# Kernel tuning notes

Hardware: AMD Instinct MI355X
Metric: run time of the kernel (lower is better)

Reference implementation:

```python
import jax, jax.numpy as jnp
import numpy as np

EMBED_DIM = 1024
NUM_HEADS = 16
HEAD_DIM = EMBED_DIM // NUM_HEADS


def setup_inputs() -> dict:
    key = jax.random.key(0)
    ks = jax.random.split(key, 9)
    B, S, E = 2, 2048, EMBED_DIM
    scale = 1.0 / np.sqrt(E)
    return {
        "query": jax.random.normal(ks[0], (B, S, E), jnp.float32),
        "key": jax.random.normal(ks[1], (B, S, E), jnp.float32),
        "value": jax.random.normal(ks[2], (B, S, E), jnp.float32),
        "wq": jax.random.normal(ks[3], (E, E), jnp.float32) * scale,
        "bq": jnp.zeros((E,), jnp.float32),
        "wk": jax.random.normal(ks[4], (E, E), jnp.float32) * scale,
        "bk": jnp.zeros((E,), jnp.float32),
        "wv": jax.random.normal(ks[5], (E, E), jnp.float32) * scale,
        "bv": jnp.zeros((E,), jnp.float32),
    }


def _split_heads(x):
    B, S, _ = x.shape
    return x.reshape(B, S, NUM_HEADS, HEAD_DIM).transpose(0, 2, 1, 3)  # [B,H,S,Dh]


def reference(query, key, value, wq, bq, wk, bk, wv, bv):
    q = _split_heads(query @ wq + bq)   # [B,H,S,Dh]
    k = _split_heads(key @ wk + bk)
    v = _split_heads(value @ wv + bv)
    logits = jnp.einsum("bhqd,bhkd->bhqk", q, k) / jnp.sqrt(
        jnp.asarray(HEAD_DIM, q.dtype)
    )
    attn = jax.nn.softmax(logits, axis=-1)          # [B,H,S,S]
    out = jnp.einsum("bhqk,bhkd->bhqd", attn, v)    # [B,H,S,Dh]
    B, H, S, Dh = out.shape
    out = out.transpose(0, 2, 1, 3).reshape(B, S, H * Dh)  # [B,S,E]
    return out, attn
```

## Files before the change

kernel.cpp:

```cpp
#include <hip/hip_runtime.h>

typedef float  f32x4   __attribute__((ext_vector_type(4)));
typedef float  f32x16  __attribute__((ext_vector_type(16)));
typedef int    i32x4   __attribute__((ext_vector_type(4)));
typedef short  bf16x8  __attribute__((ext_vector_type(8)));
typedef short  s16x4   __attribute__((ext_vector_type(4)));

#define NB   2
#define SEQ  2048
#define EMB  1024
#define NH   16
#define DH   64
#define MATN (NB * SEQ * EMB)

__device__ inline short f2bf(float f) {
    unsigned u = __float_as_uint(f);
    u += 0x7fffu + ((u >> 16) & 1u);
    return (short)(u >> 16);
}

__device__ inline unsigned cvtpk(float lo, float hi) {
    unsigned r;
    asm("v_cvt_pk_bf16_f32 %0, %1, %2" : "=v"(r) : "v"(lo), "v"(hi));
    return r;
}

__device__ inline float fexp2(float x) {
#if __has_builtin(__builtin_amdgcn_exp2f)
    return __builtin_amdgcn_exp2f(x);
#else
    return exp2f(x);
#endif
}

__device__ inline f32x4 mfma16(bf16x8 a, bf16x8 b, f32x4 c) {
    return __builtin_amdgcn_mfma_f32_16x16x32_bf16(a, b, c, 0, 0, 0);
}
__device__ inline f32x16 mfma32(bf16x8 a, bf16x8 b, f32x16 c) {
    return __builtin_amdgcn_mfma_f32_32x32x16_bf16(a, b, c, 0, 0, 0);
}

__device__ inline void gload_lds16(const short* g, short* l) {
    __builtin_amdgcn_global_load_lds(
        (const __attribute__((address_space(1))) void*)g,
        (__attribute__((address_space(3))) void*)l, 16, 0, 0);
}

__global__ __launch_bounds__(256) void prep_kernel(const float* __restrict__ q,
                                                   const float* __restrict__ k,
                                                   const float* __restrict__ v,
                                                   const float* __restrict__ w0,
                                                   const float* __restrict__ w1,
                                                   const float* __restrict__ w2,
                                                   short* __restrict__ wt,
                                                   short* __restrict__ abf) {
    int blk = blockIdx.x;
    int t = threadIdx.x;
    if (blk < 3072) {
        __shared__ float tile[32][33];
        int mat = blk >> 10;
        int rem = blk & 1023;
        int kt = rem >> 5, nt = rem & 31;
        const float* W = (mat == 0) ? w0 : ((mat == 1) ? w1 : w2);
        int row = t >> 3, c4 = (t & 7) << 2;

        f32x4 val = *(const f32x4*)(W + (kt * 32 + row) * EMB + nt * 32 + c4);
        tile[row][c4 + 0] = val[0];
        tile[row][c4 + 1] = val[1];
        tile[row][c4 + 2] = val[2];
        tile[row][c4 + 3] = val[3];
        __syncthreads();

        int n = nt * 32 + row;
        s16x4 o;
        o[0] = f2bf(tile[c4 + 0][row]);
        o[1] = f2bf(tile[c4 + 1][row]);
        o[2] = f2bf(tile[c4 + 2][row]);
        o[3] = f2bf(tile[c4 + 3][row]);
        *(s16x4*)(wt + mat * (EMB * EMB) + n * EMB + kt * 32 + c4) = o;
    } else {
        long long i = (long long)(blk - 3072) * 2048 + t * 8;
        int mat = (int)(i >> 22);
        int off = (int)(i & (MATN - 1));
        const float* A = (mat == 0) ? q : ((mat == 1) ? k : v);
        f32x4 x = *(const f32x4*)(A + off);
        f32x4 y = *(const f32x4*)(A + off + 4);
        bf16x8 pk;
        pk[0] = f2bf(x[0]); pk[1] = f2bf(x[1]); pk[2] = f2bf(x[2]); pk[3] = f2bf(x[3]);
        pk[4] = f2bf(y[0]); pk[5] = f2bf(y[1]); pk[6] = f2bf(y[2]); pk[7] = f2bf(y[3]);
        *(bf16x8*)(abf + i) = pk;
    }
}

template <bool BF16A>
__global__ __launch_bounds__(256) void proj_kernel(const short* __restrict__ abf,
                                                   const float* __restrict__ a0,
                                                   const float* __restrict__ a1,
                                                   const float* __restrict__ a2,
                                                   const float* __restrict__ b0,
                                                   const float* __restrict__ b1,
                                                   const float* __restrict__ b2,
                                                   const short* __restrict__ wt,
                                                   short* __restrict__ qkv) {
    __shared__ __align__(16) short smem[18432];

    int orig = blockIdx.x;
    int blk = (orig & 7) * 96 + (orig >> 3);
    int mat = blk >> 8;
    int rem = blk & 255;
    int mt = rem >> 3, nt = rem & 7;

    const float* bias = (mat == 0) ? b0 : ((mat == 1) ? b1 : b2);
    const float* Af = (mat == 0) ? a0 : ((mat == 1) ? a1 : a2);
    const short* Ab = abf + mat * MATN;
    const short* WT = wt + mat * (EMB * EMB);
    short* O = qkv + mat * MATN;
    float scale = (mat == 0) ? 0.125f * 1.44269504f : 1.0f;

    int t = threadIdx.x;
    int lane = t & 63, w = t >> 6;
    int wr = w >> 1, wc = w & 1;
    int lg = lane >> 4, lm = lane & 15;

    int m0 = mt * 128, n0 = nt * 128;

    f32x4 acc[4][4] = {};

    if constexpr (BF16A) {
        const short* gA[4];
        const short* gW[4];
        int ldso[4];
#pragma unroll
        for (int i = 0; i < 4; i++) {
            int u = w * 256 + i * 64 + lane;
            int row = u >> 3;
            int c = (u & 7) ^ (row & 7);
            gA[i] = Ab + (m0 + row) * EMB + c * 8;
            gW[i] = WT + (n0 + row) * EMB + c * 8;
            ldso[i] = (w * 256 + i * 64) * 8;
        }
        int xr = lm & 7;
        for (int k0 = 0; k0 < EMB; k0 += 64) {
#pragma unroll
            for (int i = 0; i < 4; i++) {
                gload_lds16(gA[i] + k0, smem + ldso[i]);
                gload_lds16(gW[i] + k0, smem + 8192 + ldso[i]);
            }
            __syncthreads();
#pragma unroll
            for (int ks = 0; ks < 2; ks++) {
                bf16x8 af[4], bfr[4];
                int cc = (ks * 4 + lg) ^ xr;
#pragma unroll
                for (int mi = 0; mi < 4; mi++)
                    af[mi] = *(const bf16x8*)(smem + (wr * 64 + mi * 16 + lm) * 64 + cc * 8);
#pragma unroll
                for (int ni = 0; ni < 4; ni++)
                    bfr[ni] = *(const bf16x8*)(smem + 8192 + (wc * 64 + ni * 16 + lm) * 64 + cc * 8);
#pragma unroll
                for (int mi = 0; mi < 4; mi++)
#pragma unroll
                    for (int ni = 0; ni < 4; ni++)
                        acc[mi][ni] = mfma16(af[mi], bfr[ni], acc[mi][ni]);
            }
            __syncthreads();
        }
    } else {
        int srow = t >> 1, koff = (t & 1) * 32;
        for (int k0 = 0; k0 < EMB; k0 += 64) {
            const float* ap = Af + (m0 + srow) * EMB + k0 + koff;
#pragma unroll
            for (int i = 0; i < 4; i++) {
                f32x4 x = *(const f32x4*)(ap + i * 8);
                f32x4 y = *(const f32x4*)(ap + i * 8 + 4);
                bf16x8 pk;
                pk[0] = f2bf(x[0]); pk[1] = f2bf(x[1]); pk[2] = f2bf(x[2]); pk[3] = f2bf(x[3]);
                pk[4] = f2bf(y[0]); pk[5] = f2bf(y[1]); pk[6] = f2bf(y[2]); pk[7] = f2bf(y[3]);
                *(bf16x8*)&smem[srow * 72 + koff + i * 8] = pk;
            }
            const short* wp = WT + (n0 + srow) * EMB + k0 + koff;
#pragma unroll
            for (int i = 0; i < 4; i++)
                *(i32x4*)&smem[9216 + srow * 72 + koff + i * 8] = *(const i32x4*)(wp + i * 8);
            __syncthreads();
#pragma unroll
            for (int ks = 0; ks < 2; ks++) {
                bf16x8 af[4], bfr[4];
#pragma unroll
                for (int mi = 0; mi < 4; mi++)
                    af[mi] = *(const bf16x8*)&smem[(wr * 64 + mi * 16 + lm) * 72 + ks * 32 + lg * 8];
#pragma unroll
                for (int ni = 0; ni < 4; ni++)
                    bfr[ni] = *(const bf16x8*)&smem[9216 + (wc * 64 + ni * 16 + lm) * 72 + ks * 32 + lg * 8];
#pragma unroll
                for (int mi = 0; mi < 4; mi++)
#pragma unroll
                    for (int ni = 0; ni < 4; ni++)
                        acc[mi][ni] = mfma16(af[mi], bfr[ni], acc[mi][ni]);
            }
            __syncthreads();
        }
    }

    int bidx = m0 >> 11;
    if (mat == 2) {
#pragma unroll
        for (int ni = 0; ni < 4; ni++) {
            int e = n0 + wc * 64 + ni * 16 + lm;
            float bv = bias[e];
            int h = e >> 6, d = e & 63;
#pragma unroll
            for (int mi = 0; mi < 4; mi++) {
                int s = (m0 + wr * 64 + mi * 16 + lg * 4) & (SEQ - 1);
                s16x4 o;
#pragma unroll
                for (int r = 0; r < 4; r++) o[r] = f2bf(acc[mi][ni][r] + bv);
                *(s16x4*)(O + (((bidx * NH + h) * DH + d) * SEQ) + s) = o;
            }
        }
    } else {
#pragma unroll
        for (int ni = 0; ni < 4; ni++) {
            int e = n0 + wc * 64 + ni * 16 + lm;
            float bv = bias[e];
#pragma unroll
            for (int mi = 0; mi < 4; mi++) {
                int rr = wr * 64 + mi * 16 + lg * 4;
#pragma unroll
                for (int r = 0; r < 4; r++)
                    smem[(rr + r) * 136 + wc * 64 + ni * 16 + lm] =
                        f2bf((acc[mi][ni][r] + bv) * scale);
            }
        }
        __syncthreads();
        int r = t >> 1, half = t & 1;
        int h = (n0 + half * 64) >> 6;
        int s = (m0 + r) & (SEQ - 1);
        short* dst = O + (((long long)bidx * NH + h) * SEQ + s) * DH;
        const short* srcp = smem + r * 136 + half * 64;
#pragma unroll
        for (int j = 0; j < 8; j++)
            *(i32x4*)(dst + j * 8) = *(const i32x4*)(srcp + j * 8);
    }
}

__global__ __launch_bounds__(256) void attn_kernel(const short* __restrict__ qkv,
                                                   float* __restrict__ out,
                                                   float* __restrict__ attn) {
    const short* Qb = qkv;
    const short* Kb = qkv + MATN;
    const short* Vt = qkv + 2 * MATN;

    __shared__ __align__(16) short kbuf[2][64][72];
    __shared__ __align__(16) short vbuf[2][4096];
    __shared__ float lds_rs[4][32];

    int orig = blockIdx.x;
    int wg = (orig & 7) * 128 + (orig >> 3);
    int bh = wg >> 5;
    int q0 = (wg & 31) * 64;
    int b = bh >> 4, hq = bh & 15;

    int t = threadIdx.x, lane = t & 63, w = t >> 6;
    int lg = lane >> 4, lm = lane & 15;
    int srow = t >> 2, sch = t & 3;

    const short* kbase = Kb + (long long)bh * SEQ * DH;
    const short* vbase = Vt + (long long)bh * DH * SEQ;

    bf16x8 qf0, qf1;
    {
        const short* qrow = Qb + ((long long)bh * SEQ + q0 + w * 16 + lm) * DH + lg * 8;
        qf0 = *(const bf16x8*)(qrow);
        qf1 = *(const bf16x8*)(qrow + 32);
    }

    int l31 = lane & 31, l5 = lane >> 5;
    int khalf = w >> 1;
    bf16x8 qw[4];
    {
        const short* qr = Qb + ((long long)bh * SEQ + q0 + (w & 1) * 32 + l31) * DH + l5 * 8;
        qw[0] = *(const bf16x8*)(qr);
        qw[1] = *(const bf16x8*)(qr + 16);
        qw[2] = *(const bf16x8*)(qr + 32);
        qw[3] = *(const bf16x8*)(qr + 48);
    }

    i32x4 kr0, kr1;
    {
        const short* kp = kbase + srow * DH + sch * 16;
        kr0 = *(const i32x4*)(kp); kr1 = *(const i32x4*)(kp + 8);
    }
    float rsum = 0.0f;
    for (int kt = 0; kt < 32; kt++) {
        *(i32x4*)&kbuf[kt & 1][srow][sch * 16]     = kr0;
        *(i32x4*)&kbuf[kt & 1][srow][sch * 16 + 8] = kr1;
        __syncthreads();
        if (kt < 31) {
            const short* kp = kbase + ((kt + 1) * 64 + srow) * DH + sch * 16;
            kr0 = *(const i32x4*)(kp); kr1 = *(const i32x4*)(kp + 8);
        }
        const short* kb = &kbuf[kt & 1][khalf * 32 + l31][l5 * 8];
        f32x16 s = {};
        __builtin_amdgcn_s_setprio(1);
        s = mfma32(*(const bf16x8*)(kb),      qw[0], s);
        s = mfma32(*(const bf16x8*)(kb + 16), qw[1], s);
        s = mfma32(*(const bf16x8*)(kb + 32), qw[2], s);
        s = mfma32(*(const bf16x8*)(kb + 48), qw[3], s);
        __builtin_amdgcn_s_setprio(0);
#pragma unroll
        for (int r = 0; r < 16; r++) rsum += fexp2(s[r]);
    }
    rsum += __shfl_xor(rsum, 32);
    if (lane < 32) lds_rs[w][lane] = rsum;
    __syncthreads();
    float ml2r;
    {
        int q = w * 16 + lm;
        float tot = (q < 32) ? (lds_rs[0][q] + lds_rs[2][q])
                             : (lds_rs[1][q - 32] + lds_rs[3][q - 32]);
        ml2r = -__log2f(tot);
    }

    f32x4 oacc[4] = {};
    float* arow = attn + ((long long)bh * SEQ + q0 + w * 16 + lm) * SEQ;

    int vA0 = (srow >> 4) * 1024 + (sch >> 1) * 512 + (srow & 15) * 8 + (sch & 1) * 4;

    i32x4 vr0, vr1;
    {
        const short* kp = kbase + srow * DH + sch * 16;
        kr0 = *(const i32x4*)(kp); kr1 = *(const i32x4*)(kp + 8);
        const short* vp = vbase + srow * SEQ + sch * 16;
        vr0 = *(const i32x4*)(vp); vr1 = *(const i32x4*)(vp + 8);
    }

    for (int kt = 0; kt < 32; kt++) {
        *(i32x4*)&kbuf[kt & 1][srow][sch * 16]     = kr0;
        *(i32x4*)&kbuf[kt & 1][srow][sch * 16 + 8] = kr1;
        union { i32x4 v; s16x4 h[2]; } u0, u1;
        u0.v = vr0; u1.v = vr1;
        *(s16x4*)&vbuf[kt & 1][vA0]       = u0.h[0];
        *(s16x4*)&vbuf[kt & 1][vA0 + 128] = u0.h[1];
        *(s16x4*)&vbuf[kt & 1][vA0 + 256] = u1.h[0];
        *(s16x4*)&vbuf[kt & 1][vA0 + 384] = u1.h[1];
        __syncthreads();
        if (kt < 31) {
            const short* kp = kbase + ((kt + 1) * 64 + srow) * DH + sch * 16;
            kr0 = *(const i32x4*)(kp); kr1 = *(const i32x4*)(kp + 8);
            const short* vp = vbase + srow * SEQ + (kt + 1) * 64 + sch * 16;
            vr0 = *(const i32x4*)(vp); vr1 = *(const i32x4*)(vp + 8);
        }

        float p[4][4];
#pragma unroll
        for (int ki = 0; ki < 4; ki++) {
            f32x4 s = {ml2r, ml2r, ml2r, ml2r};
            bf16x8 kf0 = *(const bf16x8*)&kbuf[kt & 1][ki * 16 + lm][lg * 8];
            bf16x8 kf1 = *(const bf16x8*)&kbuf[kt & 1][ki * 16 + lm][32 + lg * 8];
            __builtin_amdgcn_s_setprio(1);
            s = mfma16(kf0, qf0, s);
            s = mfma16(kf1, qf1, s);
            __builtin_amdgcn_s_setprio(0);
#pragma unroll
            for (int r = 0; r < 4; r++) p[ki][r] = fexp2(s[r]);
            f32x4 st = {p[ki][0], p[ki][1], p[ki][2], p[ki][3]};
            __builtin_nontemporal_store(st, (f32x4*)(arow + kt * 64 + ki * 16 + lg * 4));
        }

        bf16x8 pb[2];
#pragma unroll
        for (int ks = 0; ks < 2; ks++) {
            union { unsigned d[4]; bf16x8 v; } up;
            up.d[0] = cvtpk(p[2 * ks + 0][0], p[2 * ks + 0][1]);
            up.d[1] = cvtpk(p[2 * ks + 0][2], p[2 * ks + 0][3]);
            up.d[2] = cvtpk(p[2 * ks + 1][0], p[2 * ks + 1][1]);
            up.d[3] = cvtpk(p[2 * ks + 1][2], p[2 * ks + 1][3]);
            pb[ks] = up.v;
        }

        __builtin_amdgcn_s_setprio(1);
#pragma unroll
        for (int di = 0; di < 4; di++) {
#pragma unroll
            for (int ks = 0; ks < 2; ks++) {
                bf16x8 vf = *(const bf16x8*)&vbuf[kt & 1][(di * 2 + ks) * 512 + (lg * 16 + lm) * 8];
                oacc[di] = mfma16(vf, pb[ks], oacc[di]);
            }
        }
        __builtin_amdgcn_s_setprio(0);
    }

    float* op = out + ((long long)b * SEQ + q0 + w * 16 + lm) * EMB + hq * DH;
#pragma unroll
    for (int di = 0; di < 4; di++) {
        __builtin_nontemporal_store(oacc[di], (f32x4*)(op + di * 16 + lg * 4));
    }
}

extern "C" void kernel_launch(void* const* d_in, const int* in_sizes, int n_in,
                              void* d_out, int out_size, void* d_ws, size_t ws_size,
                              hipStream_t stream) {
    const float* query = (const float*)d_in[0];
    const float* key   = (const float*)d_in[1];
    const float* value = (const float*)d_in[2];
    const float* wq    = (const float*)d_in[3];
    const float* bq    = (const float*)d_in[4];
    const float* wk    = (const float*)d_in[5];
    const float* bk    = (const float*)d_in[6];
    const float* wv    = (const float*)d_in[7];
    const float* bv    = (const float*)d_in[8];

    float* out  = (float*)d_out;
    float* attn = out + (long long)NB * SEQ * EMB;

    size_t need_full = ((size_t)3 * EMB * EMB + 6ull * MATN) * sizeof(short);
    bool bf16a = ws_size >= need_full;

    short* wt  = (short*)d_ws;
    short* abf = wt + 3 * (EMB * EMB);
    short* qkv = bf16a ? (abf + 3 * MATN) : abf;

    hipLaunchKernelGGL(prep_kernel, dim3(bf16a ? 9216 : 3072), dim3(256), 0, stream,
                       query, key, value, wq, wk, wv, wt, abf);
    if (bf16a) {
        hipLaunchKernelGGL((proj_kernel<true>), dim3(768), dim3(256), 0, stream,
                           abf, query, key, value, bq, bk, bv, wt, qkv);
    } else {
        hipLaunchKernelGGL((proj_kernel<false>), dim3(768), dim3(256), 0, stream,
                           abf, query, key, value, bq, bk, bv, wt, qkv);
    }
    hipLaunchKernelGGL(attn_kernel, dim3(1024), dim3(256), 0, stream,
                       qkv, out, attn);
}
```

Measured before the change: 258.2 us.

## Switch attention output pass to 32x32 MFMA tiles with split-K merge via LDS

The second pass, which computes scores and P@V, now uses 32x32x16 MFMA instead of 16x16x32. Each wave handles a 32-query by 32-key quadrant, and the V tile layout in LDS is changed to match. The two key-half waves each hold partial output accumulators, which are merged through LDS at the end before the final store. The intent is fewer MFMA and LDS-read instructions per tile, reusing the Q fragments already loaded for the first pass. In exchange it adds an extra merge step with two barriers, and changes the attention store pattern to 32-column quadrant strips.

After: 485.0 us. 1.88x slower.

```diff
diff --git a/kernel.cpp b/kernel.cpp
--- a/kernel.cpp
+++ b/kernel.cpp
@@ -262,24 +262,16 @@
     int b = bh >> 4, hq = bh & 15;
 
     int t = threadIdx.x, lane = t & 63, w = t >> 6;
-    int lg = lane >> 4, lm = lane & 15;
     int srow = t >> 2, sch = t & 3;
+    int l31 = lane & 31, l5 = lane >> 5;
+    int qh = w & 1, kh = w >> 1;
 
     const short* kbase = Kb + (long long)bh * SEQ * DH;
     const short* vbase = Vt + (long long)bh * DH * SEQ;
 
-    bf16x8 qf0, qf1;
-    {
-        const short* qrow = Qb + ((long long)bh * SEQ + q0 + w * 16 + lm) * DH + lg * 8;
-        qf0 = *(const bf16x8*)(qrow);
-        qf1 = *(const bf16x8*)(qrow + 32);
-    }
-
-    int l31 = lane & 31, l5 = lane >> 5;
-    int khalf = w >> 1;
     bf16x8 qw[4];
     {
-        const short* qr = Qb + ((long long)bh * SEQ + q0 + (w & 1) * 32 + l31) * DH + l5 * 8;
+        const short* qr = Qb + ((long long)bh * SEQ + q0 + qh * 32 + l31) * DH + l5 * 8;
         qw[0] = *(const bf16x8*)(qr);
         qw[1] = *(const bf16x8*)(qr + 16);
         qw[2] = *(const bf16x8*)(qr + 32);
@@ -300,7 +292,7 @@
             const short* kp = kbase + ((kt + 1) * 64 + srow) * DH + sch * 16;
             kr0 = *(const i32x4*)(kp); kr1 = *(const i32x4*)(kp + 8);
         }
-        const short* kb = &kbuf[kt & 1][khalf * 32 + l31][l5 * 8];
+        const short* kb = &kbuf[kt & 1][kh * 32 + l31][l5 * 8];
         f32x16 s = {};
         __builtin_amdgcn_s_setprio(1);
         s = mfma32(*(const bf16x8*)(kb),      qw[0], s);
@@ -314,18 +306,13 @@
     rsum += __shfl_xor(rsum, 32);
     if (lane < 32) lds_rs[w][lane] = rsum;
     __syncthreads();
-    float ml2r;
-    {
-        int q = w * 16 + lm;
-        float tot = (q < 32) ? (lds_rs[0][q] + lds_rs[2][q])
-                             : (lds_rs[1][q - 32] + lds_rs[3][q - 32]);
-        ml2r = -__log2f(tot);
-    }
-
-    f32x4 oacc[4] = {};
-    float* arow = attn + ((long long)bh * SEQ + q0 + w * 16 + lm) * SEQ;
-
-    int vA0 = (srow >> 4) * 1024 + (sch >> 1) * 512 + (srow & 15) * 8 + (sch & 1) * 4;
+    float ml2r = -__log2f(lds_rs[qh][l31] + lds_rs[2 + qh][l31]);
+
+    f32x16 acc2[2] = {};
+    float* arow2 = attn + ((long long)bh * SEQ + q0 + qh * 32 + l31) * SEQ + kh * 32;
+
+    int vidx = ((sch >> 1) * 2 + (sch & 1)) * 2 + (srow >> 5);
+    int vA = vidx * 512 + (srow & 31) * 8;
 
     i32x4 vr0, vr1;
     {
@@ -340,10 +327,10 @@
         *(i32x4*)&kbuf[kt & 1][srow][sch * 16 + 8] = kr1;
         union { i32x4 v; s16x4 h[2]; } u0, u1;
         u0.v = vr0; u1.v = vr1;
-        *(s16x4*)&vbuf[kt & 1][vA0]       = u0.h[0];
-        *(s16x4*)&vbuf[kt & 1][vA0 + 128] = u0.h[1];
-        *(s16x4*)&vbuf[kt & 1][vA0 + 256] = u1.h[0];
-        *(s16x4*)&vbuf[kt & 1][vA0 + 384] = u1.h[1];
+        *(s16x4*)&vbuf[kt & 1][vA]       = u0.h[0];
+        *(s16x4*)&vbuf[kt & 1][vA + 256] = u0.h[1];
+        *(s16x4*)&vbuf[kt & 1][vA + 4]   = u1.h[0];
+        *(s16x4*)&vbuf[kt & 1][vA + 260] = u1.h[1];
         __syncthreads();
         if (kt < 31) {
             const short* kp = kbase + ((kt + 1) * 64 + srow) * DH + sch * 16;
@@ -352,49 +339,78 @@
             vr0 = *(const i32x4*)(vp); vr1 = *(const i32x4*)(vp + 8);
         }
 
-        float p[4][4];
-#pragma unroll
-        for (int ki = 0; ki < 4; ki++) {
-            f32x4 s = {ml2r, ml2r, ml2r, ml2r};
-            bf16x8 kf0 = *(const bf16x8*)&kbuf[kt & 1][ki * 16 + lm][lg * 8];
-            bf16x8 kf1 = *(const bf16x8*)&kbuf[kt & 1][ki * 16 + lm][32 + lg * 8];
-            __builtin_amdgcn_s_setprio(1);
-            s = mfma16(kf0, qf0, s);
-            s = mfma16(kf1, qf1, s);
-            __builtin_amdgcn_s_setprio(0);
-#pragma unroll
-            for (int r = 0; r < 4; r++) p[ki][r] = fexp2(s[r]);
-            f32x4 st = {p[ki][0], p[ki][1], p[ki][2], p[ki][3]};
-            __builtin_nontemporal_store(st, (f32x4*)(arow + kt * 64 + ki * 16 + lg * 4));
+        const short* kb2 = &kbuf[kt & 1][kh * 32 + l31][l5 * 8];
+        f32x16 s;
+#pragma unroll
+        for (int r = 0; r < 16; r++) s[r] = ml2r;
+        __builtin_amdgcn_s_setprio(1);
+        s = mfma32(*(const bf16x8*)(kb2),      qw[0], s);
+        s = mfma32(*(const bf16x8*)(kb2 + 16), qw[1], s);
+        s = mfma32(*(const bf16x8*)(kb2 + 32), qw[2], s);
+        s = mfma32(*(const bf16x8*)(kb2 + 48), qw[3], s);
+        __builtin_amdgcn_s_setprio(0);
+
+        float p[16];
+#pragma unroll
+        for (int rg = 0; rg < 4; rg++) {
+            f32x4 st;
+#pragma unroll
+            for (int j = 0; j < 4; j++) {
+                float e = fexp2(s[rg * 4 + j]);
+                p[rg * 4 + j] = e;
+                st[j] = e;
+            }
+            __builtin_nontemporal_store(st, (f32x4*)(arow2 + kt * 64 + rg * 8 + l5 * 4));
         }
 
         bf16x8 pb[2];
 #pragma unroll
-        for (int ks = 0; ks < 2; ks++) {
+        for (int c = 0; c < 2; c++) {
             union { unsigned d[4]; bf16x8 v; } up;
-            up.d[0] = cvtpk(p[2 * ks + 0][0], p[2 * ks + 0][1]);
-            up.d[1] = cvtpk(p[2 * ks + 0][2], p[2 * ks + 0][3]);
-            up.d[2] = cvtpk(p[2 * ks + 1][0], p[2 * ks + 1][1]);
-            up.d[3] = cvtpk(p[2 * ks + 1][2], p[2 * ks + 1][3]);
-            pb[ks] = up.v;
+            up.d[0] = cvtpk(p[c * 8 + 0], p[c * 8 + 1]);
+            up.d[1] = cvtpk(p[c * 8 + 2], p[c * 8 + 3]);
+            up.d[2] = cvtpk(p[c * 8 + 4], p[c * 8 + 5]);
+            up.d[3] = cvtpk(p[c * 8 + 6], p[c * 8 + 7]);
+            pb[c] = up.v;
         }
 
         __builtin_amdgcn_s_setprio(1);
 #pragma unroll
-        for (int di = 0; di < 4; di++) {
-#pragma unroll
-            for (int ks = 0; ks < 2; ks++) {
-                bf16x8 vf = *(const bf16x8*)&vbuf[kt & 1][(di * 2 + ks) * 512 + (lg * 16 + lm) * 8];
-                oacc[di] = mfma16(vf, pb[ks], oacc[di]);
+        for (int db = 0; db < 2; db++) {
+#pragma unroll
+            for (int c = 0; c < 2; c++) {
+                bf16x8 vf = *(const bf16x8*)&vbuf[kt & 1]
+                    [((kh * 2 + c) * 2 + db) * 512 + l5 * 256 + l31 * 8];
+                acc2[db] = mfma32(vf, pb[c], acc2[db]);
             }
         }
         __builtin_amdgcn_s_setprio(0);
     }
 
-    float* op = out + ((long long)b * SEQ + q0 + w * 16 + lm) * EMB + hq * DH;
-#pragma unroll
-    for (int di = 0; di < 4; di++) {
-        __builtin_nontemporal_store(oacc[di], (f32x4*)(op + di * 16 + lg * 4));
+    __syncthreads();
+    float* mrg = (float*)&kbuf[0][0][0];
+    if (kh == 1) {
+#pragma unroll
+        for (int db = 0; db < 2; db++)
+#pragma unroll
+            for (int rg = 0; rg < 4; rg++) {
+                f32x4 v = {acc2[db][rg * 4 + 0], acc2[db][rg * 4 + 1],
+                           acc2[db][rg * 4 + 2], acc2[db][rg * 4 + 3]};
+                *(f32x4*)&mrg[((qh * 2 + db) * 4 + rg) * 256 + lane * 4] = v;
+            }
+    }
+    __syncthreads();
+    if (kh == 0) {
+        float* op2 = out + ((long long)b * SEQ + q0 + qh * 32 + l31) * EMB + hq * DH;
+#pragma unroll
+        for (int db = 0; db < 2; db++)
+#pragma unroll
+            for (int rg = 0; rg < 4; rg++) {
+                f32x4 m = *(const f32x4*)&mrg[((qh * 2 + db) * 4 + rg) * 256 + lane * 4];
+                f32x4 o = {acc2[db][rg * 4 + 0] + m[0], acc2[db][rg * 4 + 1] + m[1],
+                           acc2[db][rg * 4 + 2] + m[2], acc2[db][rg * 4 + 3] + m[3]};
+                __builtin_nontemporal_store(o, (f32x4*)(op2 + db * 32 + rg * 8 + l5 * 4));
+            }
     }
 }
 
```
